# Kernel optimization log

Measured on AMD Instinct MI355X. Metric: run time of the kernel, lower is better.

Reference implementation:

```python
import jax, jax.numpy as jnp
import numpy as np

N_EMBD = 1024
N_HEAD = 16
D_HEAD = N_EMBD // N_HEAD
B, T = 4, 2048


def _layernorm(x, g, b, eps=1e-5):
    mu = jnp.mean(x, axis=-1, keepdims=True)
    var = jnp.var(x, axis=-1, keepdims=True)
    return (x - mu) * jax.lax.rsqrt(var + eps) * g + b


def setup_inputs() -> dict:
    key = jax.random.key(0)
    ks = jax.random.split(key, 16)
    C = N_EMBD
    s = 0.02
    return {
        "x": jax.random.normal(ks[0], (B, T, C), jnp.float32),
        "ln1_g": jnp.ones((C,), jnp.float32),
        "ln1_b": jnp.zeros((C,), jnp.float32),
        "Wq": jax.random.normal(ks[1], (C, C), jnp.float32) * s,
        "bq": jnp.zeros((C,), jnp.float32),
        "Wk": jax.random.normal(ks[2], (C, C), jnp.float32) * s,
        "bk": jnp.zeros((C,), jnp.float32),
        "Wv": jax.random.normal(ks[3], (C, C), jnp.float32) * s,
        "bv": jnp.zeros((C,), jnp.float32),
        "Wo": jax.random.normal(ks[4], (C, C), jnp.float32) * s,
        "bo": jnp.zeros((C,), jnp.float32),
        "ln2_g": jnp.ones((C,), jnp.float32),
        "ln2_b": jnp.zeros((C,), jnp.float32),
        "W1": jax.random.normal(ks[5], (C, 4 * C), jnp.float32) * s,
        "b1": jnp.zeros((4 * C,), jnp.float32),
        "W2": jax.random.normal(ks[6], (4 * C, C), jnp.float32) * s,
        "b2": jnp.zeros((C,), jnp.float32),
    }


def reference(x, ln1_g, ln1_b, Wq, bq, Wk, bk, Wv, bv, Wo, bo,
              ln2_g, ln2_b, W1, b1, W2, b2):
    Bx, Tx, C = x.shape
    H, D = N_HEAD, D_HEAD

    # --- attention (pre-LN) ---
    h = _layernorm(x, ln1_g, ln1_b)
    q = (h @ Wq + bq).reshape(Bx, Tx, H, D)
    k = (h @ Wk + bk).reshape(Bx, Tx, H, D)
    v = (h @ Wv + bv).reshape(Bx, Tx, H, D)
    att = jnp.einsum("bqhd,bkhd->bhqk", q, k) * (1.0 / jnp.sqrt(jnp.float32(D)))
    causal = jnp.tril(jnp.ones((Tx, Tx), bool))
    att = jnp.where(causal, att, -jnp.inf)
    att = jax.nn.softmax(att, axis=-1)
    y = jnp.einsum("bhqk,bkhd->bqhd", att, v).reshape(Bx, Tx, C)
    x = x + (y @ Wo + bo)

    # --- MLP (pre-LN), exact GELU as in torch F.gelu default ---
    h2 = _layernorm(x, ln2_g, ln2_b)
    m = jax.nn.gelu(h2 @ W1 + b1, approximate=False)
    x = x + (m @ W2 + b2)
    return x
```

## Files before the change

kernel.cpp:

```cpp
#include <hip/hip_runtime.h>
#include <hip/hip_bf16.h>
#include <math.h>

#define C_EMBD 1024
#define T_SEQ  2048
#define BATCH  4
#define NHEAD  16
#define DHEAD  64

typedef __attribute__((ext_vector_type(8))) short bf16x8;
typedef __attribute__((ext_vector_type(4))) float floatx4;

#if __has_builtin(__builtin_amdgcn_exp2f)
#define EXP2F __builtin_amdgcn_exp2f
#else
#define EXP2F exp2f
#endif

static __device__ __forceinline__ floatx4 mfma16(bf16x8 a, bf16x8 b, floatx4 c) {
    return __builtin_amdgcn_mfma_f32_16x16x32_bf16(a, b, c, 0, 0, 0);
}

static __device__ __forceinline__ void gl2lds16(const void* g, void* l) {
    __builtin_amdgcn_global_load_lds(
        (const __attribute__((address_space(1))) void*)g,
        (__attribute__((address_space(3))) void*)l, 16, 0, 0);
}

__global__ __launch_bounds__(256) void transpose_cvt(
        const float* __restrict__ W, __hip_bfloat16* __restrict__ Wt, int K, int N) {
    __shared__ float tile[32][33];
    const int tid = threadIdx.x;
    const int n0 = blockIdx.x * 32, k0 = blockIdx.y * 32;
    const int r = tid >> 3, c4 = (tid & 7) * 4;
    float4 v = *(const float4*)&W[(size_t)(k0 + r) * N + n0 + c4];
    tile[r][c4 + 0] = v.x; tile[r][c4 + 1] = v.y;
    tile[r][c4 + 2] = v.z; tile[r][c4 + 3] = v.w;
    __syncthreads();
    __align__(8) __hip_bfloat16 ob[4];
    ob[0] = __float2bfloat16(tile[c4 + 0][r]);
    ob[1] = __float2bfloat16(tile[c4 + 1][r]);
    ob[2] = __float2bfloat16(tile[c4 + 2][r]);
    ob[3] = __float2bfloat16(tile[c4 + 3][r]);
    *(short4*)&Wt[(size_t)(n0 + r) * K + k0 + c4] = *(short4*)ob;
}

__global__ __launch_bounds__(256) void ln_bf16(
        const float* __restrict__ x, const float* __restrict__ g,
        const float* __restrict__ b, __hip_bfloat16* __restrict__ out) {
    const int row = blockIdx.x, tid = threadIdx.x;
    const float4 v = ((const float4*)(x + (size_t)row * C_EMBD))[tid];
    float s  = v.x + v.y + v.z + v.w;
    float sq = v.x * v.x + v.y * v.y + v.z * v.z + v.w * v.w;
    #pragma unroll
    for (int off = 1; off < 64; off <<= 1) {
        s  += __shfl_xor(s, off);
        sq += __shfl_xor(sq, off);
    }
    __shared__ float ps[4], pq[4];
    if ((tid & 63) == 0) { ps[tid >> 6] = s; pq[tid >> 6] = sq; }
    __syncthreads();
    s  = ps[0] + ps[1] + ps[2] + ps[3];
    sq = pq[0] + pq[1] + pq[2] + pq[3];
    const float mu   = s * (1.0f / C_EMBD);
    const float var  = sq * (1.0f / C_EMBD) - mu * mu;
    const float rstd = rsqrtf(var + 1e-5f);
    const float4 gv = ((const float4*)g)[tid];
    const float4 bv = ((const float4*)b)[tid];
    __align__(8) __hip_bfloat16 ob[4];
    ob[0] = __float2bfloat16((v.x - mu) * rstd * gv.x + bv.x);
    ob[1] = __float2bfloat16((v.y - mu) * rstd * gv.y + bv.y);
    ob[2] = __float2bfloat16((v.z - mu) * rstd * gv.z + bv.z);
    ob[3] = __float2bfloat16((v.w - mu) * rstd * gv.w + bv.w);
    *(short4*)&out[(size_t)row * C_EMBD + tid * 4] = *(short4*)ob;
}

template <int EP>
__global__ __launch_bounds__(256, 2) void gemm_bt(
        const __hip_bfloat16* __restrict__ A, const __hip_bfloat16* __restrict__ Bt,
        int M, int N, int K,
        const float* __restrict__ ba, const float* __restrict__ bb, const float* __restrict__ bc,
        __hip_bfloat16* __restrict__ o0, __hip_bfloat16* __restrict__ o1,
        __hip_bfloat16* __restrict__ o2, float* __restrict__ of,
        const float* __restrict__ resid) {
    __shared__ __align__(16) __hip_bfloat16 As[2][128 * 32];
    __shared__ __align__(16) __hip_bfloat16 Bs[2][128 * 32];
    const int tid  = threadIdx.x;

    const int gx  = gridDim.x;
    const int nwg = gx * gridDim.y;
    const int lin = blockIdx.x + gx * blockIdx.y;
    const int cpx = nwg >> 3;
    const int wg  = (lin & 7) * cpx + (lin >> 3);
    const int by  = (wg & 7) + 8 * (wg / (gx << 3));
    const int bx  = (wg >> 3) % gx;
    const int n0  = bx * 128;
    const int m0  = by * 128;

    const int wave = tid >> 6, lane = tid & 63;
    const int l15  = lane & 15, quad = lane >> 4;
    const int wm   = (wave & 1) * 64, wn = (wave >> 1) * 64;
    const int c0   = wave * 2;
    const int sr   = lane >> 2;
    const int sc   = (lane & 3) * 8;

    const floatx4 z4 = {0.f, 0.f, 0.f, 0.f};
    floatx4 acc[4][4];
    #pragma unroll
    for (int i = 0; i < 4; i++)
        #pragma unroll
        for (int j = 0; j < 4; j++) acc[i][j] = z4;

    auto stage = [&](const int buf, const int k0) {
        gl2lds16(&A [(m0 + c0 * 16 + sr) * K + k0 + sc],       &As[buf][c0 * 512]);
        gl2lds16(&A [(m0 + (c0 + 1) * 16 + sr) * K + k0 + sc], &As[buf][(c0 + 1) * 512]);
        gl2lds16(&Bt[(n0 + c0 * 16 + sr) * K + k0 + sc],       &Bs[buf][c0 * 512]);
        gl2lds16(&Bt[(n0 + (c0 + 1) * 16 + sr) * K + k0 + sc], &Bs[buf][(c0 + 1) * 512]);
    };

    stage(0, 0);
    asm volatile("s_waitcnt vmcnt(0)" ::: "memory");
    __builtin_amdgcn_s_barrier();
    asm volatile("" ::: "memory");

    const int nk = K >> 5;
    int cur = 0;
    for (int t = 0; t < nk; ++t) {
        if (t + 1 < nk) stage(cur ^ 1, (t + 1) * 32);
        bf16x8 af[4], bfr[4];
        #pragma unroll
        for (int i = 0; i < 4; i++)
            af[i] = *(const bf16x8*)&As[cur][(wm + i * 16 + l15) * 32 + quad * 8];
        #pragma unroll
        for (int j = 0; j < 4; j++)
            bfr[j] = *(const bf16x8*)&Bs[cur][(wn + j * 16 + l15) * 32 + quad * 8];
        #pragma unroll
        for (int i = 0; i < 4; i++)
            #pragma unroll
            for (int j = 0; j < 4; j++)
                acc[i][j] = mfma16(af[i], bfr[j], acc[i][j]);
        asm volatile("s_waitcnt lgkmcnt(0) vmcnt(0)" ::: "memory");
        __builtin_amdgcn_s_barrier();
        asm volatile("" ::: "memory");
        cur ^= 1;
    }

    #pragma unroll
    for (int i = 0; i < 4; i++) {
        #pragma unroll
        for (int j = 0; j < 4; j++) {
            const int col = n0 + wn + j * 16 + l15;
            #pragma unroll
            for (int r = 0; r < 4; r++) {
                const int m = m0 + wm + i * 16 + quad * 4 + r;
                float val = acc[i][j][r];
                if (EP == 0) {
                    const int which = col >> 10, cn = col & 1023;
                    const float* bp = (which == 0) ? ba : (which == 1) ? bb : bc;
                    val += bp[cn];
                    const int head = cn >> 6, d = cn & 63;
                    const int bidx = m >> 11, t = m & 2047;
                    if (which == 0) {
                        val *= 0.18033688011112042f;
                        o0[((bidx * NHEAD + head) * T_SEQ + t) * DHEAD + d] = __float2bfloat16(val);
                    } else if (which == 1) {
                        o1[((bidx * NHEAD + head) * T_SEQ + t) * DHEAD + d] = __float2bfloat16(val);
                    } else {
                        o2[((bidx * NHEAD + head) * DHEAD + d) * T_SEQ + t] = __float2bfloat16(val);
                    }
                } else if (EP == 1) {
                    val += ba[col];
                    of[m * N + col] = resid[m * N + col] + val;
                } else if (EP == 2) {
                    val += ba[col];
                    const float gl = 0.5f * val * (1.0f + erff(val * 0.70710678118654752f));
                    o0[m * N + col] = __float2bfloat16(gl);
                } else {
                    val += ba[col];
                    of[m * N + col] += val;
                }
            }
        }
    }
}

__global__ __launch_bounds__(256, 2) void attn_fa(
        const __hip_bfloat16* __restrict__ q, const __hip_bfloat16* __restrict__ k,
        const __hip_bfloat16* __restrict__ vt, __hip_bfloat16* __restrict__ y) {
    __shared__ __align__(16) __hip_bfloat16 Ks[2][64 * 64];
    __shared__ __align__(16) __hip_bfloat16 Vs[2][64 * 64];
    __shared__ __align__(16) __hip_bfloat16 pl[4][32 * 72];
    const int tid = threadIdx.x;
    const int wave = tid >> 6, lane = tid & 63;
    const int l15 = lane & 15, quad = lane >> 4;
    const int sw  = l15 & 7;
    const int lr  = lane >> 3;
    const int gsw = (lane & 7) ^ lr;

    const int lin  = blockIdx.x;
    const int xcd  = lin & 7;
    const int slot = lin >> 3;
    const int bh   = xcd * 8 + (slot >> 3);
    const int jA   = slot & 7;

    const __hip_bfloat16* qp = q + (size_t)bh * T_SEQ * DHEAD;
    const __hip_bfloat16* kp = k + (size_t)bh * T_SEQ * DHEAD;
    const __hip_bfloat16* vp = vt + (size_t)bh * DHEAD * T_SEQ;
    __hip_bfloat16* myp = &pl[wave][0];
    const int b = bh >> 4, head = bh & 15;
    const floatx4 z4 = {0.f, 0.f, 0.f, 0.f};

    auto stage = [&](const int buf, const int kb) {
        #pragma unroll
        for (int j = 0; j < 2; j++) {
            const int rb = wave * 16 + j * 8;
            gl2lds16(&kp[(size_t)(kb + rb + lr) * DHEAD + gsw * 8], &Ks[buf][rb * 64]);
            gl2lds16(&vp[(size_t)(rb + lr) * T_SEQ + kb + gsw * 8], &Vs[buf][rb * 64]);
        }
    };

    auto segment = [&](const int tile) {
        const int q0 = tile * 128;
        const int qw = q0 + wave * 32;
        const int cc = tile * 2 + 1;

        bf16x8 bq[2][2];
        #pragma unroll
        for (int qi = 0; qi < 2; qi++)
            #pragma unroll
            for (int h = 0; h < 2; h++)
                bq[qi][h] = *(const bf16x8*)&qp[(qw + qi * 16 + l15) * DHEAD + h * 32 + quad * 8];

        floatx4 oac[2][4];
        #pragma unroll
        for (int qi = 0; qi < 2; qi++)
            #pragma unroll
            for (int nd = 0; nd < 4; nd++) oac[qi][nd] = z4;
        float li[2] = {0.f, 0.f};

        stage(0, 0);

        for (int t = 0; t <= cc; t++) {
            const int cur = t & 1;
            if (t < cc) {
                stage(cur ^ 1, (t + 1) * 64);
                asm volatile("s_waitcnt vmcnt(4)" ::: "memory");
            } else {
                asm volatile("s_waitcnt vmcnt(0)" ::: "memory");
            }
            __builtin_amdgcn_s_barrier();
            asm volatile("" ::: "memory");

            const int kb = t * 64;
            const bool act = (kb <= qw + 31);
            if (act) {
                const bool dg = (kb + 63 > qw);
                bf16x8 kf[4][2];
                #pragma unroll
                for (int nt = 0; nt < 4; nt++)
                    #pragma unroll
                    for (int h = 0; h < 2; h++)
                        kf[nt][h] = *(const bf16x8*)&Ks[cur][(nt * 16 + l15) * 64 + (((h * 4 + quad) ^ sw) * 8)];
                floatx4 sa[2][4];
                #pragma unroll
                for (int qi = 0; qi < 2; qi++)
                    #pragma unroll
                    for (int nt = 0; nt < 4; nt++) sa[qi][nt] = z4;
                #pragma unroll
                for (int nt = 0; nt < 4; nt++)
                    #pragma unroll
                    for (int h = 0; h < 2; h++) {
                        sa[0][nt] = mfma16(kf[nt][h], bq[0][h], sa[0][nt]);
                        sa[1][nt] = mfma16(kf[nt][h], bq[1][h], sa[1][nt]);
                    }
                if (dg) {
                    #pragma unroll
                    for (int qi = 0; qi < 2; qi++)
                        #pragma unroll
                        for (int nt = 0; nt < 4; nt++)
                            #pragma unroll
                            for (int r = 0; r < 4; r++)
                                if (kb + nt * 16 + quad * 4 + r > qw + qi * 16 + l15)
                                    sa[qi][nt][r] = -INFINITY;
                }
                #pragma unroll
                for (int qi = 0; qi < 2; qi++) {
                    float sm = 0.f;
                    #pragma unroll
                    for (int nt = 0; nt < 4; nt++) {
                        __align__(8) __hip_bfloat16 pk[4];
                        #pragma unroll
                        for (int r = 0; r < 4; r++) {
                            const float p = EXP2F(sa[qi][nt][r]);
                            sm += p;
                            pk[r] = __float2bfloat16(p);
                        }
                        *(short4*)&myp[(qi * 16 + l15) * 72 + nt * 16 + quad * 4] = *(short4*)pk;
                    }
                    li[qi] += sm;
                }
                bf16x8 vf[4][2];
                #pragma unroll
                for (int nd = 0; nd < 4; nd++)
                    #pragma unroll
                    for (int kh = 0; kh < 2; kh++)
                        vf[nd][kh] = *(const bf16x8*)&Vs[cur][(nd * 16 + l15) * 64 + (((kh * 4 + quad) ^ sw) * 8)];
                asm volatile("s_waitcnt lgkmcnt(0)" ::: "memory");
                bf16x8 pf[2][2];
                #pragma unroll
                for (int qi = 0; qi < 2; qi++)
                    #pragma unroll
                    for (int kh = 0; kh < 2; kh++)
                        pf[qi][kh] = *(const bf16x8*)&myp[(qi * 16 + l15) * 72 + kh * 32 + quad * 8];
                #pragma unroll
                for (int nd = 0; nd < 4; nd++)
                    #pragma unroll
                    for (int kh = 0; kh < 2; kh++) {
                        oac[0][nd] = mfma16(vf[nd][kh], pf[0][kh], oac[0][nd]);
                        oac[1][nd] = mfma16(vf[nd][kh], pf[1][kh], oac[1][nd]);
                    }
            }
            asm volatile("" ::: "memory");
            __builtin_amdgcn_s_barrier();
        }

        float inv[2];
        #pragma unroll
        for (int qi = 0; qi < 2; qi++) {
            float l = li[qi];
            l += __shfl_xor(l, 16);
            l += __shfl_xor(l, 32);
            inv[qi] = 1.0f / l;
        }
        #pragma unroll
        for (int qi = 0; qi < 2; qi++)
            #pragma unroll
            for (int nd = 0; nd < 4; nd++) {
                __align__(8) __hip_bfloat16 ok[4];
                #pragma unroll
                for (int r = 0; r < 4; r++) ok[r] = __float2bfloat16(oac[qi][nd][r] * inv[qi]);
                *(short4*)&myp[(qi * 16 + l15) * 72 + nd * 16 + quad * 4] = *(short4*)ok;
            }
        asm volatile("s_waitcnt lgkmcnt(0)" ::: "memory");
        #pragma unroll
        for (int half = 0; half < 2; half++) {
            const int row = half * 16 + (lane >> 2);
            const int cb  = (lane & 3) * 16;
            const bf16x8 v0 = *(const bf16x8*)&myp[row * 72 + cb];
            const bf16x8 v1 = *(const bf16x8*)&myp[row * 72 + cb + 8];
            __hip_bfloat16* yr = &y[(size_t)(b * T_SEQ + qw + row) * C_EMBD + head * DHEAD + cb];
            *(bf16x8*)yr       = v0;
            *(bf16x8*)(yr + 8) = v1;
        }
        asm volatile("s_waitcnt vmcnt(0)" ::: "memory");
    };

    segment(jA);
    segment(15 - jA);
}

extern "C" void kernel_launch(void* const* d_in, const int* in_sizes, int n_in,
                              void* d_out, int out_size, void* d_ws, size_t ws_size,
                              hipStream_t stream) {
    const float* x     = (const float*)d_in[0];
    const float* ln1_g = (const float*)d_in[1];
    const float* ln1_b = (const float*)d_in[2];
    const float* Wq    = (const float*)d_in[3];
    const float* bq    = (const float*)d_in[4];
    const float* Wk    = (const float*)d_in[5];
    const float* bk    = (const float*)d_in[6];
    const float* Wv    = (const float*)d_in[7];
    const float* bv    = (const float*)d_in[8];
    const float* Wo    = (const float*)d_in[9];
    const float* bo    = (const float*)d_in[10];
    const float* ln2_g = (const float*)d_in[11];
    const float* ln2_b = (const float*)d_in[12];
    const float* W1    = (const float*)d_in[13];
    const float* b1    = (const float*)d_in[14];
    const float* W2    = (const float*)d_in[15];
    const float* b2    = (const float*)d_in[16];
    float* out = (float*)d_out;

    char* ws = (char*)d_ws;
    __hip_bfloat16* wqkvt = (__hip_bfloat16*)(ws);
    __hip_bfloat16* wot   = (__hip_bfloat16*)(ws + 6291456);
    __hip_bfloat16* w1t   = (__hip_bfloat16*)(ws + 8388608);
    __hip_bfloat16* w2t   = (__hip_bfloat16*)(ws + 16777216);
    __hip_bfloat16* hbuf  = (__hip_bfloat16*)(ws + 25165824);
    __hip_bfloat16* qbuf  = (__hip_bfloat16*)(ws + 41943040);
    __hip_bfloat16* kbuf  = (__hip_bfloat16*)(ws + 58720256);
    __hip_bfloat16* vbuf  = (__hip_bfloat16*)(ws + 75497472);
    __hip_bfloat16* ybuf  = (__hip_bfloat16*)(ws + 92274688);
    __hip_bfloat16* mbuf  = (__hip_bfloat16*)(ws + 41943040);

    transpose_cvt<<<dim3(32, 32), 256, 0, stream>>>(Wq, wqkvt, 1024, 1024);
    transpose_cvt<<<dim3(32, 32), 256, 0, stream>>>(Wk, wqkvt + 1024 * 1024, 1024, 1024);
    transpose_cvt<<<dim3(32, 32), 256, 0, stream>>>(Wv, wqkvt + 2048 * 1024, 1024, 1024);
    transpose_cvt<<<dim3(32, 32), 256, 0, stream>>>(Wo, wot, 1024, 1024);
    transpose_cvt<<<dim3(128, 32), 256, 0, stream>>>(W1, w1t, 1024, 4096);
    transpose_cvt<<<dim3(32, 128), 256, 0, stream>>>(W2, w2t, 4096, 1024);

    ln_bf16<<<8192, 256, 0, stream>>>(x, ln1_g, ln1_b, hbuf);

    gemm_bt<0><<<dim3(24, 64), 256, 0, stream>>>(hbuf, wqkvt, 8192, 3072, 1024,
        bq, bk, bv, qbuf, kbuf, vbuf, nullptr, nullptr);

    attn_fa<<<dim3(512), 256, 0, stream>>>(qbuf, kbuf, vbuf, ybuf);

    gemm_bt<1><<<dim3(8, 64), 256, 0, stream>>>(ybuf, wot, 8192, 1024, 1024,
        bo, nullptr, nullptr, nullptr, nullptr, nullptr, out, x);

    ln_bf16<<<8192, 256, 0, stream>>>(out, ln2_g, ln2_b, hbuf);

    gemm_bt<2><<<dim3(32, 64), 256, 0, stream>>>(hbuf, w1t, 8192, 4096, 1024,
        b1, nullptr, nullptr, mbuf, nullptr, nullptr, nullptr, nullptr);

    gemm_bt<3><<<dim3(8, 64), 256, 0, stream>>>(mbuf, w2t, 8192, 1024, 4096,
        b2, nullptr, nullptr, nullptr, nullptr, nullptr, out, nullptr);
}
```

Before: 549.6 us.

## Add 256x256-tile GELU GEMM for MLP up-projection and relax GEMM pipeline waits

Adds a new 512-thread kernel with 256x256 output tiles, XCD-aware block remapping and swizzled LDS layout for the W1 GELU GEMM. It replaces the 128x128 generic kernel for that stage. Separately, the generic GEMM loop now waits with a partial vmcnt so the next stage's loads stay in flight while the current tile computes. The larger tiles raise register pressure and lower occupancy, and the loose waitcnt relies on the exact count of outstanding loads.

```diff
diff --git a/kernel.cpp b/kernel.cpp
--- a/kernel.cpp
+++ b/kernel.cpp
@@ -119,14 +119,17 @@
     };
 
     stage(0, 0);
-    asm volatile("s_waitcnt vmcnt(0)" ::: "memory");
-    __builtin_amdgcn_s_barrier();
-    asm volatile("" ::: "memory");
-
     const int nk = K >> 5;
-    int cur = 0;
     for (int t = 0; t < nk; ++t) {
-        if (t + 1 < nk) stage(cur ^ 1, (t + 1) * 32);
+        const int cur = t & 1;
+        if (t + 1 < nk) {
+            stage(cur ^ 1, (t + 1) * 32);
+            asm volatile("s_waitcnt vmcnt(4)" ::: "memory");
+        } else {
+            asm volatile("s_waitcnt vmcnt(0)" ::: "memory");
+        }
+        __builtin_amdgcn_s_barrier();
+        asm volatile("" ::: "memory");
         bf16x8 af[4], bfr[4];
         #pragma unroll
         for (int i = 0; i < 4; i++)
@@ -139,10 +142,8 @@
             #pragma unroll
             for (int j = 0; j < 4; j++)
                 acc[i][j] = mfma16(af[i], bfr[j], acc[i][j]);
-        asm volatile("s_waitcnt lgkmcnt(0) vmcnt(0)" ::: "memory");
+        asm volatile("" ::: "memory");
         __builtin_amdgcn_s_barrier();
-        asm volatile("" ::: "memory");
-        cur ^= 1;
     }
 
     #pragma unroll
@@ -184,6 +185,91 @@
     }
 }
 
+__global__ __launch_bounds__(512, 2) void gemm256_gelu(
+        const __hip_bfloat16* __restrict__ A, const __hip_bfloat16* __restrict__ Bt,
+        int M, int N, int K, const float* __restrict__ ba,
+        __hip_bfloat16* __restrict__ o0) {
+    __shared__ __align__(16) __hip_bfloat16 As[2][256 * 32];
+    __shared__ __align__(16) __hip_bfloat16 Bs[2][256 * 32];
+    const int tid = threadIdx.x;
+
+    const int gx  = gridDim.x;
+    const int nwg = gx * gridDim.y;
+    const int lin = blockIdx.x + gx * blockIdx.y;
+    const int cpx = nwg >> 3;
+    const int wg  = (lin & 7) * cpx + (lin >> 3);
+    const int by  = (wg & 7) + 8 * (wg / (gx << 3));
+    const int bx  = (wg >> 3) % gx;
+    const int n0  = bx * 256;
+    const int m0  = by * 256;
+
+    const int wave = tid >> 6, lane = tid & 63;
+    const int l15  = lane & 15, quad = lane >> 4;
+    const int wm   = (wave & 1) * 128;
+    const int wn   = (wave >> 1) * 64;
+    const int lr   = lane >> 2;
+    const int gsw  = (lane & 3) ^ (lr & 3);
+    const int sw   = l15 & 3;
+
+    const floatx4 z4 = {0.f, 0.f, 0.f, 0.f};
+    floatx4 acc[8][4];
+    #pragma unroll
+    for (int i = 0; i < 8; i++)
+        #pragma unroll
+        for (int j = 0; j < 4; j++) acc[i][j] = z4;
+
+    auto stage = [&](const int buf, const int k0) {
+        #pragma unroll
+        for (int j = 0; j < 2; j++) {
+            const int rb = wave * 32 + j * 16;
+            gl2lds16(&A [(size_t)(m0 + rb + lr) * K + k0 + gsw * 8], &As[buf][rb * 32]);
+            gl2lds16(&Bt[(size_t)(n0 + rb + lr) * K + k0 + gsw * 8], &Bs[buf][rb * 32]);
+        }
+    };
+
+    stage(0, 0);
+    const int nk = K >> 5;
+    for (int t = 0; t < nk; ++t) {
+        const int cur = t & 1;
+        if (t + 1 < nk) {
+            stage(cur ^ 1, (t + 1) * 32);
+            asm volatile("s_waitcnt vmcnt(4)" ::: "memory");
+        } else {
+            asm volatile("s_waitcnt vmcnt(0)" ::: "memory");
+        }
+        __builtin_amdgcn_s_barrier();
+        asm volatile("" ::: "memory");
+        bf16x8 bfr[4];
+        #pragma unroll
+        for (int nj = 0; nj < 4; nj++)
+            bfr[nj] = *(const bf16x8*)&Bs[cur][(wn + nj * 16 + l15) * 32 + ((quad ^ sw) * 8)];
+        #pragma unroll
+        for (int mi = 0; mi < 8; mi++) {
+            const bf16x8 afa = *(const bf16x8*)&As[cur][(wm + mi * 16 + l15) * 32 + ((quad ^ sw) * 8)];
+            #pragma unroll
+            for (int nj = 0; nj < 4; nj++)
+                acc[mi][nj] = mfma16(afa, bfr[nj], acc[mi][nj]);
+        }
+        asm volatile("" ::: "memory");
+        __builtin_amdgcn_s_barrier();
+    }
+
+    #pragma unroll
+    for (int mi = 0; mi < 8; mi++)
+        #pragma unroll
+        for (int nj = 0; nj < 4; nj++) {
+            const int col = n0 + wn + nj * 16 + l15;
+            const float bias = ba[col];
+            #pragma unroll
+            for (int r = 0; r < 4; r++) {
+                const int m = m0 + wm + mi * 16 + quad * 4 + r;
+                float val = acc[mi][nj][r] + bias;
+                const float gl = 0.5f * val * (1.0f + erff(val * 0.70710678118654752f));
+                o0[(size_t)m * N + col] = __float2bfloat16(gl);
+            }
+        }
+}
+
 __global__ __launch_bounds__(256, 2) void attn_fa(
         const __hip_bfloat16* __restrict__ q, const __hip_bfloat16* __restrict__ k,
         const __hip_bfloat16* __restrict__ vt, __hip_bfloat16* __restrict__ y) {
@@ -412,8 +498,8 @@
 
     ln_bf16<<<8192, 256, 0, stream>>>(out, ln2_g, ln2_b, hbuf);
 
-    gemm_bt<2><<<dim3(32, 64), 256, 0, stream>>>(hbuf, w1t, 8192, 4096, 1024,
-        b1, nullptr, nullptr, mbuf, nullptr, nullptr, nullptr, nullptr);
+    gemm256_gelu<<<dim3(16, 32), 512, 0, stream>>>(hbuf, w1t, 8192, 4096, 1024,
+        b1, mbuf);
 
     gemm_bt<3><<<dim3(8, 64), 256, 0, stream>>>(mbuf, w2t, 8192, 1024, 4096,
         b2, nullptr, nullptr, nullptr, nullptr, nullptr, out, nullptr);
```

New measurement: 548.2 us. Within noise of the previous version (-0.3%).
